# Kernel tuning notes

Hardware: AMD Instinct MI355X
Metric: run time of the kernel (lower is better)

## Reference

```python
import jax, jax.numpy as jnp
import numpy as np

N = 100000
E = 1600000
IN_DIM = 64
HID = 64


def _glorot(key, shape):
    fan_in, fan_out = shape[0], shape[1]
    lim = np.sqrt(6.0 / (fan_in + fan_out))
    return jax.random.uniform(key, shape, jnp.float32, -lim, lim)


def setup_inputs() -> dict:
    key = jax.random.key(0)
    ks = jax.random.split(key, 14)
    x = jax.random.normal(ks[0], (N, IN_DIM), jnp.float32)
    edge_index = jax.random.randint(ks[1], (2, E), 0, N, jnp.int64)
    dims = [(IN_DIM, HID), (HID, HID), (HID, HID), (HID, 1)]
    inp = {"x": x, "edge_index": edge_index}
    for i, (di, do) in enumerate(dims, start=1):
        inp[f"Wself{i}"] = _glorot(ks[2 + 3 * (i - 1)], (di, do))
        inp[f"Wneigh{i}"] = _glorot(ks[3 + 3 * (i - 1)], (di, do))
        inp[f"b{i}"] = jnp.zeros((do,), jnp.float32)
    return inp


def _gn_block(h, src, dst, deg_inv, Wself, Wneigh, b, act):
    # gather -> scatter-add -> mean -> dense transform (GraphConv-style)
    msg = h[src]                                           # [E, d]
    agg = jax.ops.segment_sum(msg, dst, num_segments=N)    # [N, d]
    agg = agg * deg_inv                                    # mean aggregation
    out = h @ Wself + agg @ Wneigh + b
    return act(out)


def reference(x, edge_index, Wself1, Wneigh1, b1, Wself2, Wneigh2, b2,
              Wself3, Wneigh3, b3, Wself4, Wneigh4, b4):
    src, dst = edge_index[0], edge_index[1]
    deg = jax.ops.segment_sum(jnp.ones((E,), x.dtype), dst, num_segments=N)
    deg_inv = (1.0 / jnp.maximum(deg, 1.0))[:, None]       # [N, 1]
    relu = jax.nn.relu
    h = _gn_block(x, src, dst, deg_inv, Wself1, Wneigh1, b1, relu)
    h = _gn_block(h, src, dst, deg_inv, Wself2, Wneigh2, b2, relu)
    h = _gn_block(h, src, dst, deg_inv, Wself3, Wneigh3, b3, relu)
    h = _gn_block(h, src, dst, deg_inv, Wself4, Wneigh4, b4, lambda z: z)
    return jax.nn.sigmoid(h)                               # [N, 1]
```

## Files before the change

### kernel.cpp

```cpp
#include <hip/hip_runtime.h>
#include <hip/hip_bf16.h>
#include <math.h>


using bfrag = __attribute__((ext_vector_type(8))) short;
using ffrag = __attribute__((ext_vector_type(4))) float;

#define BKT_SHIFT 7
#define BKT_NODES (1 << BKT_SHIFT)

__device__ __forceinline__ int load_idx32(const int* __restrict__ ei32, int is64,
                                          long long pos) {
    return is64 ? ei32[2 * pos] : ei32[pos];
}

__device__ __forceinline__ unsigned short f2b_rne(float f) {
    union { float f; unsigned u; } c;
    c.f = f;
    unsigned r = c.u + 0x7FFFu + ((c.u >> 16) & 1u);
    return (unsigned short)(r >> 16);
}

__device__ __forceinline__ float b2f(unsigned short u) {
    union { unsigned u; float f; } c;
    c.u = ((unsigned)u) << 16;
    return c.f;
}

__global__ void prep_kernel(
    const float* __restrict__ Ws1, const float* __restrict__ Wn1,
    const float* __restrict__ Ws2, const float* __restrict__ Wn2,
    const float* __restrict__ Ws3, const float* __restrict__ Wn3,
    unsigned short* __restrict__ bthi, unsigned short* __restrict__ btlo,
    const int* __restrict__ ei, int* __restrict__ bktc, int* __restrict__ flag,
    const float4* __restrict__ x4, ushort4* __restrict__ hi4, int n4) {
    int bid = blockIdx.x;
    if (bid < 96) {
        if (bid < 4) bktc[bid * 256 + threadIdx.x] = 0;
        if (bid == 0 && threadIdx.x == 0) {
            int allz = 1;
            for (int i = 0; i < 32; ++i)
                if (ei[2 * i + 1] != 0) allz = 0;
            *flag = allz;
        }
        int i = bid * 256 + threadIdx.x;
        if (i < 3 * 8192) {
            int layer = i >> 13;
            int j = i & 8191;
            int n = j >> 7, k = j & 127;
            const float* Ws = layer == 0 ? Ws1 : (layer == 1 ? Ws2 : Ws3);
            const float* Wn = layer == 0 ? Wn1 : (layer == 1 ? Wn2 : Wn3);
            float v = (k < 64) ? Ws[k * 64 + n] : Wn[(k - 64) * 64 + n];
            unsigned short hi = f2b_rne(v);
            bthi[i] = hi;
            btlo[i] = f2b_rne(v - b2f(hi));
        }
    } else {
        int i = (bid - 96) * 256 + threadIdx.x;
        if (i < n4) {
            float4 v = x4[i];
            ushort4 h;
            h.x = f2b_rne(v.x); h.y = f2b_rne(v.y);
            h.z = f2b_rne(v.z); h.w = f2b_rne(v.w);
            hi4[i] = h;
        }
    }
}

__global__ __launch_bounds__(256) void binA_kernel(
    const int* __restrict__ ei32, const int* __restrict__ flagp,
    int* __restrict__ bktCnt, unsigned* __restrict__ bins, int E, int nbkt,
    int cap, int chunksz) {
    __shared__ int cnt[1024];
    __shared__ int base[1024];
    int is64 = *flagp;
    int elo = blockIdx.x * chunksz;
    int ehi = min(E, elo + chunksz);
    if (elo >= E) return;
    for (int i = threadIdx.x; i < nbkt; i += 256) cnt[i] = 0;
    __syncthreads();
    for (int e = elo + (int)threadIdx.x; e < ehi; e += 256) {
        int dst = load_idx32(ei32, is64, (long long)E + e);
        atomicAdd(&cnt[dst >> BKT_SHIFT], 1);
    }
    __syncthreads();
    for (int i = threadIdx.x; i < nbkt; i += 256) {
        base[i] = atomicAdd(&bktCnt[i], cnt[i]);
        cnt[i] = 0;
    }
    __syncthreads();
    for (int e = elo + (int)threadIdx.x; e < ehi; e += 256) {
        int dst = load_idx32(ei32, is64, (long long)E + e);
        int src = load_idx32(ei32, is64, e);
        int b = dst >> BKT_SHIFT;
        int r = atomicAdd(&cnt[b], 1);
        bins[(size_t)b * cap + base[b] + r] =
            ((unsigned)(dst & (BKT_NODES - 1)) << 24) | (unsigned)src;
    }
}

__global__ __launch_bounds__(256) void bucketCSR_kernel(
    const int* __restrict__ bktCnt, const unsigned* __restrict__ bins,
    int* __restrict__ off, int* __restrict__ offe, int* __restrict__ col,
    float* __restrict__ dinv, int N, int cap) {
    __shared__ int deg[BKT_NODES];
    __shared__ int loc[BKT_NODES];
    __shared__ int ssum[BKT_NODES];
    int b = blockIdx.x;
    int lo = b << BKT_SHIFT;
    int n = min(BKT_NODES, N - lo);
    int t = threadIdx.x;
    if (t < BKT_NODES) deg[t] = 0;
    __syncthreads();
    int cnt = bktCnt[b];
    const unsigned* bb = bins + (size_t)b * cap;
    for (int i = t; i < cnt; i += 256)
        atomicAdd(&deg[bb[i] >> 24], 1);
    __syncthreads();
    if (t < BKT_NODES) ssum[t] = deg[t];
    __syncthreads();
    for (int o = 1; o < BKT_NODES; o <<= 1) {
        int v = (t >= o && t < BKT_NODES) ? ssum[t - o] : 0;
        __syncthreads();
        if (t < BKT_NODES) ssum[t] += v;
        __syncthreads();
    }
    if (t < BKT_NODES) loc[t] = ssum[t] - deg[t];
    __syncthreads();
    int base = b * cap;
    if (t < n) {
        int d = deg[t];
        off[lo + t] = base + loc[t];
        offe[lo + t] = base + loc[t] + d;
        dinv[lo + t] = 1.0f / fmaxf((float)d, 1.0f);
    }
    __syncthreads();
    for (int i = t; i < cnt; i += 256) {
        unsigned p = bb[i];
        int pos = atomicAdd(&loc[p >> 24], 1);
        col[base + pos] = (int)(p & 0xFFFFFFu);
    }
}

__global__ __launch_bounds__(256) void gather64_b16_kernel(
    const unsigned short* __restrict__ hb, const int* __restrict__ off,
    const int* __restrict__ offe, const int* __restrict__ col,
    const float* __restrict__ dinv, unsigned short* __restrict__ ghi, int N) {
    int wave = threadIdx.x >> 6;
    int lane = threadIdx.x & 63;
    int g = lane >> 4;
    int t = lane & 15;
    int n = blockIdx.x * 4 + wave;
    if (n >= N) return;
    int e = off[n], end = offe[n];
    float4 a0 = make_float4(0.f, 0.f, 0.f, 0.f);
    float4 a1 = make_float4(0.f, 0.f, 0.f, 0.f);
    float4 a2 = make_float4(0.f, 0.f, 0.f, 0.f);
    float4 a3 = make_float4(0.f, 0.f, 0.f, 0.f);
    for (; e + 16 <= end; e += 16) {
        int s0 = col[e + g];
        int s1 = col[e + 4 + g];
        int s2 = col[e + 8 + g];
        int s3 = col[e + 12 + g];
        ushort4 u0 = *(const ushort4*)&hb[(size_t)s0 * 64 + t * 4];
        ushort4 u1 = *(const ushort4*)&hb[(size_t)s1 * 64 + t * 4];
        ushort4 u2 = *(const ushort4*)&hb[(size_t)s2 * 64 + t * 4];
        ushort4 u3 = *(const ushort4*)&hb[(size_t)s3 * 64 + t * 4];
        a0.x += b2f(u0.x); a0.y += b2f(u0.y); a0.z += b2f(u0.z); a0.w += b2f(u0.w);
        a1.x += b2f(u1.x); a1.y += b2f(u1.y); a1.z += b2f(u1.z); a1.w += b2f(u1.w);
        a2.x += b2f(u2.x); a2.y += b2f(u2.y); a2.z += b2f(u2.z); a2.w += b2f(u2.w);
        a3.x += b2f(u3.x); a3.y += b2f(u3.y); a3.z += b2f(u3.z); a3.w += b2f(u3.w);
    }
    for (; e + 8 <= end; e += 8) {
        int s0 = col[e + g];
        int s1 = col[e + 4 + g];
        ushort4 u0 = *(const ushort4*)&hb[(size_t)s0 * 64 + t * 4];
        ushort4 u1 = *(const ushort4*)&hb[(size_t)s1 * 64 + t * 4];
        a0.x += b2f(u0.x); a0.y += b2f(u0.y); a0.z += b2f(u0.z); a0.w += b2f(u0.w);
        a1.x += b2f(u1.x); a1.y += b2f(u1.y); a1.z += b2f(u1.z); a1.w += b2f(u1.w);
    }
    for (; e < end; e += 4) {
        if (e + g < end) {
            int s0 = col[e + g];
            ushort4 u0 = *(const ushort4*)&hb[(size_t)s0 * 64 + t * 4];
            a2.x += b2f(u0.x); a2.y += b2f(u0.y); a2.z += b2f(u0.z); a2.w += b2f(u0.w);
        }
    }
    float4 acc;
    acc.x = (a0.x + a1.x) + (a2.x + a3.x);
    acc.y = (a0.y + a1.y) + (a2.y + a3.y);
    acc.z = (a0.z + a1.z) + (a2.z + a3.z);
    acc.w = (a0.w + a1.w) + (a2.w + a3.w);
#pragma unroll
    for (int m = 16; m <= 32; m <<= 1) {
        acc.x += __shfl_xor(acc.x, m, 64);
        acc.y += __shfl_xor(acc.y, m, 64);
        acc.z += __shfl_xor(acc.z, m, 64);
        acc.w += __shfl_xor(acc.w, m, 64);
    }
    if (g == 0) {
        float di = dinv[n];
        ushort4 h;
        h.x = f2b_rne(acc.x * di);
        h.y = f2b_rne(acc.y * di);
        h.z = f2b_rne(acc.z * di);
        h.w = f2b_rne(acc.w * di);
        *(ushort4*)&ghi[(size_t)n * 64 + t * 4] = h;
    }
}

__global__ __launch_bounds__(256) void dense_mfma_kernel(
    const unsigned short* __restrict__ Hhi, const unsigned short* __restrict__ Ghi,
    const unsigned short* __restrict__ Bthi, const unsigned short* __restrict__ Btlo,
    const float* __restrict__ b, unsigned short* __restrict__ Dhi, int N) {
    int lane = threadIdx.x & 63;
    int m = lane & 15, quad = lane >> 4;
    int wid = (blockIdx.x * blockDim.x + threadIdx.x) >> 6;
    int nw = (gridDim.x * blockDim.x) >> 6;
    bfrag bhi[4][4];
#pragma unroll
    for (int t = 0; t < 4; ++t)
#pragma unroll
        for (int c = 0; c < 4; ++c)
            bhi[t][c] = *(const bfrag*)(Bthi + (size_t)(t * 16 + m) * 128 + c * 32 + quad * 8);
    float bl[4];
#pragma unroll
    for (int t = 0; t < 4; ++t) bl[t] = b[t * 16 + m];
    int ngroups = (N + 15) >> 4;
    for (int g = wid; g < ngroups; g += nw) {
        int n0 = g << 4;
        int nr = n0 + m;
        if (nr > N - 1) nr = N - 1;
        const unsigned short* hrow = Hhi + (size_t)nr * 64 + quad * 8;
        const unsigned short* grow = Ghi + (size_t)nr * 64 + quad * 8;
        bfrag ah[4];
        ah[0] = *(const bfrag*)(hrow);
        ah[1] = *(const bfrag*)(hrow + 32);
        ah[2] = *(const bfrag*)(grow);
        ah[3] = *(const bfrag*)(grow + 32);
#pragma unroll
        for (int t = 0; t < 4; ++t) {
            ffrag acc = {bl[t], bl[t], bl[t], bl[t]};
#pragma unroll
            for (int c = 0; c < 4; ++c) {
                bfrag blo = *(const bfrag*)(Btlo + (size_t)(t * 16 + m) * 128 + c * 32 + quad * 8);
                acc = __builtin_amdgcn_mfma_f32_16x16x32_bf16(ah[c], bhi[t][c], acc, 0, 0, 0);
                acc = __builtin_amdgcn_mfma_f32_16x16x32_bf16(ah[c], blo, acc, 0, 0, 0);
            }
#pragma unroll
            for (int r = 0; r < 4; ++r) {
                int node = n0 + quad * 4 + r;
                if (node < N)
                    Dhi[(size_t)node * 64 + t * 16 + m] = f2b_rne(fmaxf(acc[r], 0.f));
            }
        }
    }
}

__global__ __launch_bounds__(256) void dense_mfma_last_kernel(
    const unsigned short* __restrict__ Hhi, const unsigned short* __restrict__ Ghi,
    const unsigned short* __restrict__ Bthi, const unsigned short* __restrict__ Btlo,
    const float* __restrict__ b, const float* __restrict__ Ws4,
    const float* __restrict__ Wn4, float* __restrict__ sbuf,
    float* __restrict__ gbuf, int N) {
    int lane = threadIdx.x & 63;
    int m = lane & 15, quad = lane >> 4;
    int wid = (blockIdx.x * blockDim.x + threadIdx.x) >> 6;
    int nw = (gridDim.x * blockDim.x) >> 6;
    bfrag bhi[4][4];
#pragma unroll
    for (int t = 0; t < 4; ++t)
#pragma unroll
        for (int c = 0; c < 4; ++c)
            bhi[t][c] = *(const bfrag*)(Bthi + (size_t)(t * 16 + m) * 128 + c * 32 + quad * 8);
    float bl[4], w4s[4], w4n[4];
#pragma unroll
    for (int t = 0; t < 4; ++t) {
        bl[t] = b[t * 16 + m];
        w4s[t] = Ws4[t * 16 + m];
        w4n[t] = Wn4[t * 16 + m];
    }
    int ngroups = (N + 15) >> 4;
    for (int g = wid; g < ngroups; g += nw) {
        int n0 = g << 4;
        int nr = n0 + m;
        if (nr > N - 1) nr = N - 1;
        const unsigned short* hrow = Hhi + (size_t)nr * 64 + quad * 8;
        const unsigned short* grow = Ghi + (size_t)nr * 64 + quad * 8;
        bfrag ah[4];
        ah[0] = *(const bfrag*)(hrow);
        ah[1] = *(const bfrag*)(hrow + 32);
        ah[2] = *(const bfrag*)(grow);
        ah[3] = *(const bfrag*)(grow + 32);
        ffrag accs[4];
#pragma unroll
        for (int t = 0; t < 4; ++t) {
            ffrag acc = {bl[t], bl[t], bl[t], bl[t]};
#pragma unroll
            for (int c = 0; c < 4; ++c) {
                bfrag blo = *(const bfrag*)(Btlo + (size_t)(t * 16 + m) * 128 + c * 32 + quad * 8);
                acc = __builtin_amdgcn_mfma_f32_16x16x32_bf16(ah[c], bhi[t][c], acc, 0, 0, 0);
                acc = __builtin_amdgcn_mfma_f32_16x16x32_bf16(ah[c], blo, acc, 0, 0, 0);
            }
            accs[t] = acc;
        }
#pragma unroll
        for (int r = 0; r < 4; ++r) {
            float ps = 0.f, pg = 0.f;
#pragma unroll
            for (int t = 0; t < 4; ++t) {
                float v = fmaxf(accs[t][r], 0.f);
                ps = fmaf(v, w4s[t], ps);
                pg = fmaf(v, w4n[t], pg);
            }
#pragma unroll
            for (int mask = 1; mask <= 8; mask <<= 1) {
                ps += __shfl_xor(ps, mask, 64);
                pg += __shfl_xor(pg, mask, 64);
            }
            int node = n0 + quad * 4 + r;
            if (m == 0 && node < N) {
                sbuf[node] = ps;
                gbuf[node] = pg;
            }
        }
    }
}

__global__ void final_kernel(const float* __restrict__ s, const float* __restrict__ dinv,
                             const float* __restrict__ g, const int* __restrict__ off,
                             const int* __restrict__ offe, const int* __restrict__ col,
                             const float* __restrict__ b4, float* __restrict__ out, int N) {
    int n = blockIdx.x * blockDim.x + threadIdx.x;
    if (n >= N) return;
    float a = 0.f;
    int e = off[n], end = offe[n];
    for (; e < end; ++e) a += g[col[e]];
    float z = s[n] + dinv[n] * a + b4[0];
    out[n] = 1.0f / (1.0f + expf(-z));
}

static inline int cdiv(long long a, long long b) { return (int)((a + b - 1) / b); }

extern "C" void kernel_launch(void* const* d_in, const int* in_sizes, int n_in,
                              void* d_out, int out_size, void* d_ws, size_t ws_size,
                              hipStream_t stream) {
    const float* x   = (const float*)d_in[0];
    const int*   ei  = (const int*)d_in[1];
    const float* Ws1 = (const float*)d_in[2];
    const float* Wn1 = (const float*)d_in[3];
    const float* b1  = (const float*)d_in[4];
    const float* Ws2 = (const float*)d_in[5];
    const float* Wn2 = (const float*)d_in[6];
    const float* b2  = (const float*)d_in[7];
    const float* Ws3 = (const float*)d_in[8];
    const float* Wn3 = (const float*)d_in[9];
    const float* b3  = (const float*)d_in[10];
    const float* Ws4 = (const float*)d_in[11];
    const float* Wn4 = (const float*)d_in[12];
    const float* b4  = (const float*)d_in[13];
    float* out = (float*)d_out;

    const int N = in_sizes[0] / 64;
    const int E = in_sizes[1] / 2;

    const int nbkt = cdiv(N, BKT_NODES);
    const int cap  = E / nbkt + E / nbkt / 8 + 64;

    unsigned* bins = (unsigned*)d_ws;
    int* col = (int*)(bins + (size_t)nbkt * cap);
    unsigned short* HhiA = (unsigned short*)(col + (size_t)nbkt * cap);
    unsigned short* HhiB = HhiA + (size_t)N * 64;
    unsigned short* Ghi  = HhiB + (size_t)N * 64;
    unsigned short* Bth  = Ghi + (size_t)N * 64;
    unsigned short* Btl  = Bth + 3 * 8192;
    float* dinv = (float*)(Btl + 3 * 8192);
    float* sbuf = dinv + N;
    float* gbuf = sbuf + N;
    int*   off  = (int*)(gbuf + N);
    int*   offe = off + N;
    int*   bktc = offe + N;
    int*   flag = bktc + 1024;

    const int BT = 256;
    const int gridN  = cdiv(N, BT);
    const int gridNd = cdiv(N, 4);
    const int gridMM = cdiv(cdiv(N, 16), 4);
    const int binBlocks = 256;
    const int chunksz = cdiv(E, binBlocks);
    const int gridPrep = 96 + cdiv((long long)N * 16, BT);

    prep_kernel<<<gridPrep, BT, 0, stream>>>(Ws1, Wn1, Ws2, Wn2, Ws3, Wn3,
                                             Bth, Btl, ei, bktc, flag,
                                             (const float4*)x, (ushort4*)HhiA, N * 16);

    binA_kernel<<<binBlocks, BT, 0, stream>>>(ei, flag, bktc, bins, E, nbkt, cap, chunksz);
    bucketCSR_kernel<<<nbkt, BT, 0, stream>>>(bktc, bins, off, offe, col, dinv, N, cap);

    gather64_b16_kernel<<<gridNd, BT, 0, stream>>>(HhiA, off, offe, col, dinv, Ghi, N);
    dense_mfma_kernel<<<gridMM, BT, 0, stream>>>(HhiA, Ghi, Bth, Btl, b1, HhiB, N);

    gather64_b16_kernel<<<gridNd, BT, 0, stream>>>(HhiB, off, offe, col, dinv, Ghi, N);
    dense_mfma_kernel<<<gridMM, BT, 0, stream>>>(HhiB, Ghi, Bth + 8192, Btl + 8192,
                                                 b2, HhiA, N);

    gather64_b16_kernel<<<gridNd, BT, 0, stream>>>(HhiA, off, offe, col, dinv, Ghi, N);
    dense_mfma_last_kernel<<<gridMM, BT, 0, stream>>>(HhiA, Ghi, Bth + 16384,
                                                      Btl + 16384, b3, Ws4, Wn4,
                                                      sbuf, gbuf, N);

    final_kernel<<<gridN, BT, 0, stream>>>(sbuf, dinv, gbuf, off, offe, col, b4, out, N);
}
```

Before: 404.9 us.

## Fuse all stages into one cooperative persistent kernel with grid syncs

Replaces the nine separate kernel launches (prep, binning, CSR build, three gather/dense pairs, final) with a single cooperative persistent kernel that separates phases with grid.sync() and uses grid-stride loops. It also stops holding the hi bf16 weight fragments in registers across the loop and reloads them per tile, which lowers register pressure so more blocks can be resident. The aim is to remove launch gaps and tail effects between stages. In exchange, parallelism is capped at the resident block count, binning uses at most 256 blocks, and the weight reloads add memory traffic.

```diff
diff --git a/kernel.cpp b/kernel.cpp
--- a/kernel.cpp
+++ b/kernel.cpp
@@ -1,6 +1,9 @@
 #include <hip/hip_runtime.h>
 #include <hip/hip_bf16.h>
+#include <hip/hip_cooperative_groups.h>
 #include <math.h>
+
+namespace cg = cooperative_groups;
 
 
 using bfrag = __attribute__((ext_vector_type(8))) short;
@@ -8,6 +11,7 @@
 
 #define BKT_SHIFT 7
 #define BKT_NODES (1 << BKT_SHIFT)
+#define BINB 256
 
 __device__ __forceinline__ int load_idx32(const int* __restrict__ ei32, int is64,
                                           long long pos) {
@@ -27,208 +31,79 @@
     return c.f;
 }
 
-__global__ void prep_kernel(
-    const float* __restrict__ Ws1, const float* __restrict__ Wn1,
-    const float* __restrict__ Ws2, const float* __restrict__ Wn2,
-    const float* __restrict__ Ws3, const float* __restrict__ Wn3,
-    unsigned short* __restrict__ bthi, unsigned short* __restrict__ btlo,
-    const int* __restrict__ ei, int* __restrict__ bktc, int* __restrict__ flag,
-    const float4* __restrict__ x4, ushort4* __restrict__ hi4, int n4) {
-    int bid = blockIdx.x;
-    if (bid < 96) {
-        if (bid < 4) bktc[bid * 256 + threadIdx.x] = 0;
-        if (bid == 0 && threadIdx.x == 0) {
-            int allz = 1;
-            for (int i = 0; i < 32; ++i)
-                if (ei[2 * i + 1] != 0) allz = 0;
-            *flag = allz;
-        }
-        int i = bid * 256 + threadIdx.x;
-        if (i < 3 * 8192) {
-            int layer = i >> 13;
-            int j = i & 8191;
-            int n = j >> 7, k = j & 127;
-            const float* Ws = layer == 0 ? Ws1 : (layer == 1 ? Ws2 : Ws3);
-            const float* Wn = layer == 0 ? Wn1 : (layer == 1 ? Wn2 : Wn3);
-            float v = (k < 64) ? Ws[k * 64 + n] : Wn[(k - 64) * 64 + n];
-            unsigned short hi = f2b_rne(v);
-            bthi[i] = hi;
-            btlo[i] = f2b_rne(v - b2f(hi));
-        }
-    } else {
-        int i = (bid - 96) * 256 + threadIdx.x;
-        if (i < n4) {
-            float4 v = x4[i];
-            ushort4 h;
-            h.x = f2b_rne(v.x); h.y = f2b_rne(v.y);
-            h.z = f2b_rne(v.z); h.w = f2b_rne(v.w);
-            hi4[i] = h;
-        }
-    }
-}
-
-__global__ __launch_bounds__(256) void binA_kernel(
-    const int* __restrict__ ei32, const int* __restrict__ flagp,
-    int* __restrict__ bktCnt, unsigned* __restrict__ bins, int E, int nbkt,
-    int cap, int chunksz) {
-    __shared__ int cnt[1024];
-    __shared__ int base[1024];
-    int is64 = *flagp;
-    int elo = blockIdx.x * chunksz;
-    int ehi = min(E, elo + chunksz);
-    if (elo >= E) return;
-    for (int i = threadIdx.x; i < nbkt; i += 256) cnt[i] = 0;
-    __syncthreads();
-    for (int e = elo + (int)threadIdx.x; e < ehi; e += 256) {
-        int dst = load_idx32(ei32, is64, (long long)E + e);
-        atomicAdd(&cnt[dst >> BKT_SHIFT], 1);
-    }
-    __syncthreads();
-    for (int i = threadIdx.x; i < nbkt; i += 256) {
-        base[i] = atomicAdd(&bktCnt[i], cnt[i]);
-        cnt[i] = 0;
-    }
-    __syncthreads();
-    for (int e = elo + (int)threadIdx.x; e < ehi; e += 256) {
-        int dst = load_idx32(ei32, is64, (long long)E + e);
-        int src = load_idx32(ei32, is64, e);
-        int b = dst >> BKT_SHIFT;
-        int r = atomicAdd(&cnt[b], 1);
-        bins[(size_t)b * cap + base[b] + r] =
-            ((unsigned)(dst & (BKT_NODES - 1)) << 24) | (unsigned)src;
-    }
-}
-
-__global__ __launch_bounds__(256) void bucketCSR_kernel(
-    const int* __restrict__ bktCnt, const unsigned* __restrict__ bins,
-    int* __restrict__ off, int* __restrict__ offe, int* __restrict__ col,
-    float* __restrict__ dinv, int N, int cap) {
-    __shared__ int deg[BKT_NODES];
-    __shared__ int loc[BKT_NODES];
-    __shared__ int ssum[BKT_NODES];
-    int b = blockIdx.x;
-    int lo = b << BKT_SHIFT;
-    int n = min(BKT_NODES, N - lo);
-    int t = threadIdx.x;
-    if (t < BKT_NODES) deg[t] = 0;
-    __syncthreads();
-    int cnt = bktCnt[b];
-    const unsigned* bb = bins + (size_t)b * cap;
-    for (int i = t; i < cnt; i += 256)
-        atomicAdd(&deg[bb[i] >> 24], 1);
-    __syncthreads();
-    if (t < BKT_NODES) ssum[t] = deg[t];
-    __syncthreads();
-    for (int o = 1; o < BKT_NODES; o <<= 1) {
-        int v = (t >= o && t < BKT_NODES) ? ssum[t - o] : 0;
-        __syncthreads();
-        if (t < BKT_NODES) ssum[t] += v;
-        __syncthreads();
-    }
-    if (t < BKT_NODES) loc[t] = ssum[t] - deg[t];
-    __syncthreads();
-    int base = b * cap;
-    if (t < n) {
-        int d = deg[t];
-        off[lo + t] = base + loc[t];
-        offe[lo + t] = base + loc[t] + d;
-        dinv[lo + t] = 1.0f / fmaxf((float)d, 1.0f);
-    }
-    __syncthreads();
-    for (int i = t; i < cnt; i += 256) {
-        unsigned p = bb[i];
-        int pos = atomicAdd(&loc[p >> 24], 1);
-        col[base + pos] = (int)(p & 0xFFFFFFu);
-    }
-}
-
-__global__ __launch_bounds__(256) void gather64_b16_kernel(
+__device__ __forceinline__ void gather_phase(
     const unsigned short* __restrict__ hb, const int* __restrict__ off,
     const int* __restrict__ offe, const int* __restrict__ col,
-    const float* __restrict__ dinv, unsigned short* __restrict__ ghi, int N) {
-    int wave = threadIdx.x >> 6;
-    int lane = threadIdx.x & 63;
-    int g = lane >> 4;
-    int t = lane & 15;
-    int n = blockIdx.x * 4 + wave;
-    if (n >= N) return;
-    int e = off[n], end = offe[n];
-    float4 a0 = make_float4(0.f, 0.f, 0.f, 0.f);
-    float4 a1 = make_float4(0.f, 0.f, 0.f, 0.f);
-    float4 a2 = make_float4(0.f, 0.f, 0.f, 0.f);
-    float4 a3 = make_float4(0.f, 0.f, 0.f, 0.f);
-    for (; e + 16 <= end; e += 16) {
-        int s0 = col[e + g];
-        int s1 = col[e + 4 + g];
-        int s2 = col[e + 8 + g];
-        int s3 = col[e + 12 + g];
-        ushort4 u0 = *(const ushort4*)&hb[(size_t)s0 * 64 + t * 4];
-        ushort4 u1 = *(const ushort4*)&hb[(size_t)s1 * 64 + t * 4];
-        ushort4 u2 = *(const ushort4*)&hb[(size_t)s2 * 64 + t * 4];
-        ushort4 u3 = *(const ushort4*)&hb[(size_t)s3 * 64 + t * 4];
-        a0.x += b2f(u0.x); a0.y += b2f(u0.y); a0.z += b2f(u0.z); a0.w += b2f(u0.w);
-        a1.x += b2f(u1.x); a1.y += b2f(u1.y); a1.z += b2f(u1.z); a1.w += b2f(u1.w);
-        a2.x += b2f(u2.x); a2.y += b2f(u2.y); a2.z += b2f(u2.z); a2.w += b2f(u2.w);
-        a3.x += b2f(u3.x); a3.y += b2f(u3.y); a3.z += b2f(u3.z); a3.w += b2f(u3.w);
-    }
-    for (; e + 8 <= end; e += 8) {
-        int s0 = col[e + g];
-        int s1 = col[e + 4 + g];
-        ushort4 u0 = *(const ushort4*)&hb[(size_t)s0 * 64 + t * 4];
-        ushort4 u1 = *(const ushort4*)&hb[(size_t)s1 * 64 + t * 4];
-        a0.x += b2f(u0.x); a0.y += b2f(u0.y); a0.z += b2f(u0.z); a0.w += b2f(u0.w);
-        a1.x += b2f(u1.x); a1.y += b2f(u1.y); a1.z += b2f(u1.z); a1.w += b2f(u1.w);
-    }
-    for (; e < end; e += 4) {
-        if (e + g < end) {
+    const float* __restrict__ dinv, unsigned short* __restrict__ ghi,
+    int N, int wid, int nw, int g, int t) {
+    for (int n = wid; n < N; n += nw) {
+        int e = off[n], end = offe[n];
+        float4 a0 = make_float4(0.f, 0.f, 0.f, 0.f);
+        float4 a1 = make_float4(0.f, 0.f, 0.f, 0.f);
+        float4 a2 = make_float4(0.f, 0.f, 0.f, 0.f);
+        float4 a3 = make_float4(0.f, 0.f, 0.f, 0.f);
+        for (; e + 16 <= end; e += 16) {
             int s0 = col[e + g];
+            int s1 = col[e + 4 + g];
+            int s2 = col[e + 8 + g];
+            int s3 = col[e + 12 + g];
             ushort4 u0 = *(const ushort4*)&hb[(size_t)s0 * 64 + t * 4];
-            a2.x += b2f(u0.x); a2.y += b2f(u0.y); a2.z += b2f(u0.z); a2.w += b2f(u0.w);
-        }
-    }
-    float4 acc;
-    acc.x = (a0.x + a1.x) + (a2.x + a3.x);
-    acc.y = (a0.y + a1.y) + (a2.y + a3.y);
-    acc.z = (a0.z + a1.z) + (a2.z + a3.z);
-    acc.w = (a0.w + a1.w) + (a2.w + a3.w);
-#pragma unroll
-    for (int m = 16; m <= 32; m <<= 1) {
-        acc.x += __shfl_xor(acc.x, m, 64);
-        acc.y += __shfl_xor(acc.y, m, 64);
-        acc.z += __shfl_xor(acc.z, m, 64);
-        acc.w += __shfl_xor(acc.w, m, 64);
-    }
-    if (g == 0) {
-        float di = dinv[n];
-        ushort4 h;
-        h.x = f2b_rne(acc.x * di);
-        h.y = f2b_rne(acc.y * di);
-        h.z = f2b_rne(acc.z * di);
-        h.w = f2b_rne(acc.w * di);
-        *(ushort4*)&ghi[(size_t)n * 64 + t * 4] = h;
-    }
-}
-
-__global__ __launch_bounds__(256) void dense_mfma_kernel(
+            ushort4 u1 = *(const ushort4*)&hb[(size_t)s1 * 64 + t * 4];
+            ushort4 u2 = *(const ushort4*)&hb[(size_t)s2 * 64 + t * 4];
+            ushort4 u3 = *(const ushort4*)&hb[(size_t)s3 * 64 + t * 4];
+            a0.x += b2f(u0.x); a0.y += b2f(u0.y); a0.z += b2f(u0.z); a0.w += b2f(u0.w);
+            a1.x += b2f(u1.x); a1.y += b2f(u1.y); a1.z += b2f(u1.z); a1.w += b2f(u1.w);
+            a2.x += b2f(u2.x); a2.y += b2f(u2.y); a2.z += b2f(u2.z); a2.w += b2f(u2.w);
+            a3.x += b2f(u3.x); a3.y += b2f(u3.y); a3.z += b2f(u3.z); a3.w += b2f(u3.w);
+        }
+        for (; e + 8 <= end; e += 8) {
+            int s0 = col[e + g];
+            int s1 = col[e + 4 + g];
+            ushort4 u0 = *(const ushort4*)&hb[(size_t)s0 * 64 + t * 4];
+            ushort4 u1 = *(const ushort4*)&hb[(size_t)s1 * 64 + t * 4];
+            a0.x += b2f(u0.x); a0.y += b2f(u0.y); a0.z += b2f(u0.z); a0.w += b2f(u0.w);
+            a1.x += b2f(u1.x); a1.y += b2f(u1.y); a1.z += b2f(u1.z); a1.w += b2f(u1.w);
+        }
+        for (; e < end; e += 4) {
+            if (e + g < end) {
+                int s0 = col[e + g];
+                ushort4 u0 = *(const ushort4*)&hb[(size_t)s0 * 64 + t * 4];
+                a2.x += b2f(u0.x); a2.y += b2f(u0.y); a2.z += b2f(u0.z); a2.w += b2f(u0.w);
+            }
+        }
+        float4 acc;
+        acc.x = (a0.x + a1.x) + (a2.x + a3.x);
+        acc.y = (a0.y + a1.y) + (a2.y + a3.y);
+        acc.z = (a0.z + a1.z) + (a2.z + a3.z);
+        acc.w = (a0.w + a1.w) + (a2.w + a3.w);
+#pragma unroll
+        for (int m = 16; m <= 32; m <<= 1) {
+            acc.x += __shfl_xor(acc.x, m, 64);
+            acc.y += __shfl_xor(acc.y, m, 64);
+            acc.z += __shfl_xor(acc.z, m, 64);
+            acc.w += __shfl_xor(acc.w, m, 64);
+        }
+        if (g == 0) {
+            float di = dinv[n];
+            ushort4 h;
+            h.x = f2b_rne(acc.x * di);
+            h.y = f2b_rne(acc.y * di);
+            h.z = f2b_rne(acc.z * di);
+            h.w = f2b_rne(acc.w * di);
+            *(ushort4*)&ghi[(size_t)n * 64 + t * 4] = h;
+        }
+    }
+}
+
+__device__ __forceinline__ void dense_phase(
     const unsigned short* __restrict__ Hhi, const unsigned short* __restrict__ Ghi,
     const unsigned short* __restrict__ Bthi, const unsigned short* __restrict__ Btlo,
-    const float* __restrict__ b, unsigned short* __restrict__ Dhi, int N) {
-    int lane = threadIdx.x & 63;
+    const float* __restrict__ b, unsigned short* __restrict__ Dhi,
+    int N, int wid, int nw, int lane) {
     int m = lane & 15, quad = lane >> 4;
-    int wid = (blockIdx.x * blockDim.x + threadIdx.x) >> 6;
-    int nw = (gridDim.x * blockDim.x) >> 6;
-    bfrag bhi[4][4];
-#pragma unroll
-    for (int t = 0; t < 4; ++t)
-#pragma unroll
-        for (int c = 0; c < 4; ++c)
-            bhi[t][c] = *(const bfrag*)(Bthi + (size_t)(t * 16 + m) * 128 + c * 32 + quad * 8);
-    float bl[4];
-#pragma unroll
-    for (int t = 0; t < 4; ++t) bl[t] = b[t * 16 + m];
     int ngroups = (N + 15) >> 4;
-    for (int g = wid; g < ngroups; g += nw) {
-        int n0 = g << 4;
+    for (int gg = wid; gg < ngroups; gg += nw) {
+        int n0 = gg << 4;
         int nr = n0 + m;
         if (nr > N - 1) nr = N - 1;
         const unsigned short* hrow = Hhi + (size_t)nr * 64 + quad * 8;
@@ -240,12 +115,14 @@
         ah[3] = *(const bfrag*)(grow + 32);
 #pragma unroll
         for (int t = 0; t < 4; ++t) {
-            ffrag acc = {bl[t], bl[t], bl[t], bl[t]};
+            float bl = b[t * 16 + m];
+            ffrag acc = {bl, bl, bl, bl};
 #pragma unroll
             for (int c = 0; c < 4; ++c) {
-                bfrag blo = *(const bfrag*)(Btlo + (size_t)(t * 16 + m) * 128 + c * 32 + quad * 8);
-                acc = __builtin_amdgcn_mfma_f32_16x16x32_bf16(ah[c], bhi[t][c], acc, 0, 0, 0);
-                acc = __builtin_amdgcn_mfma_f32_16x16x32_bf16(ah[c], blo, acc, 0, 0, 0);
+                bfrag bh = *(const bfrag*)(Bthi + (size_t)(t * 16 + m) * 128 + c * 32 + quad * 8);
+                bfrag bw = *(const bfrag*)(Btlo + (size_t)(t * 16 + m) * 128 + c * 32 + quad * 8);
+                acc = __builtin_amdgcn_mfma_f32_16x16x32_bf16(ah[c], bh, acc, 0, 0, 0);
+                acc = __builtin_amdgcn_mfma_f32_16x16x32_bf16(ah[c], bw, acc, 0, 0, 0);
             }
 #pragma unroll
             for (int r = 0; r < 4; ++r) {
@@ -257,32 +134,16 @@
     }
 }
 
-__global__ __launch_bounds__(256) void dense_mfma_last_kernel(
+__device__ __forceinline__ void dense_last_phase(
     const unsigned short* __restrict__ Hhi, const unsigned short* __restrict__ Ghi,
     const unsigned short* __restrict__ Bthi, const unsigned short* __restrict__ Btlo,
     const float* __restrict__ b, const float* __restrict__ Ws4,
     const float* __restrict__ Wn4, float* __restrict__ sbuf,
-    float* __restrict__ gbuf, int N) {
-    int lane = threadIdx.x & 63;
+    float* __restrict__ gbuf, int N, int wid, int nw, int lane) {
     int m = lane & 15, quad = lane >> 4;
-    int wid = (blockIdx.x * blockDim.x + threadIdx.x) >> 6;
-    int nw = (gridDim.x * blockDim.x) >> 6;
-    bfrag bhi[4][4];
-#pragma unroll
-    for (int t = 0; t < 4; ++t)
-#pragma unroll
-        for (int c = 0; c < 4; ++c)
-            bhi[t][c] = *(const bfrag*)(Bthi + (size_t)(t * 16 + m) * 128 + c * 32 + quad * 8);
-    float bl[4], w4s[4], w4n[4];
-#pragma unroll
-    for (int t = 0; t < 4; ++t) {
-        bl[t] = b[t * 16 + m];
-        w4s[t] = Ws4[t * 16 + m];
-        w4n[t] = Wn4[t * 16 + m];
-    }
     int ngroups = (N + 15) >> 4;
-    for (int g = wid; g < ngroups; g += nw) {
-        int n0 = g << 4;
+    for (int gg = wid; gg < ngroups; gg += nw) {
+        int n0 = gg << 4;
         int nr = n0 + m;
         if (nr > N - 1) nr = N - 1;
         const unsigned short* hrow = Hhi + (size_t)nr * 64 + quad * 8;
@@ -295,14 +156,22 @@
         ffrag accs[4];
 #pragma unroll
         for (int t = 0; t < 4; ++t) {
-            ffrag acc = {bl[t], bl[t], bl[t], bl[t]};
+            float bl = b[t * 16 + m];
+            ffrag acc = {bl, bl, bl, bl};
 #pragma unroll
             for (int c = 0; c < 4; ++c) {
-                bfrag blo = *(const bfrag*)(Btlo + (size_t)(t * 16 + m) * 128 + c * 32 + quad * 8);
-                acc = __builtin_amdgcn_mfma_f32_16x16x32_bf16(ah[c], bhi[t][c], acc, 0, 0, 0);
-                acc = __builtin_amdgcn_mfma_f32_16x16x32_bf16(ah[c], blo, acc, 0, 0, 0);
+                bfrag bh = *(const bfrag*)(Bthi + (size_t)(t * 16 + m) * 128 + c * 32 + quad * 8);
+                bfrag bw = *(const bfrag*)(Btlo + (size_t)(t * 16 + m) * 128 + c * 32 + quad * 8);
+                acc = __builtin_amdgcn_mfma_f32_16x16x32_bf16(ah[c], bh, acc, 0, 0, 0);
+                acc = __builtin_amdgcn_mfma_f32_16x16x32_bf16(ah[c], bw, acc, 0, 0, 0);
             }
             accs[t] = acc;
+        }
+        float w4s[4], w4n[4];
+#pragma unroll
+        for (int t = 0; t < 4; ++t) {
+            w4s[t] = Ws4[t * 16 + m];
+            w4n[t] = Wn4[t * 16 + m];
         }
 #pragma unroll
         for (int r = 0; r < 4; ++r) {
@@ -327,17 +196,157 @@
     }
 }
 
-__global__ void final_kernel(const float* __restrict__ s, const float* __restrict__ dinv,
-                             const float* __restrict__ g, const int* __restrict__ off,
-                             const int* __restrict__ offe, const int* __restrict__ col,
-                             const float* __restrict__ b4, float* __restrict__ out, int N) {
-    int n = blockIdx.x * blockDim.x + threadIdx.x;
-    if (n >= N) return;
-    float a = 0.f;
-    int e = off[n], end = offe[n];
-    for (; e < end; ++e) a += g[col[e]];
-    float z = s[n] + dinv[n] * a + b4[0];
-    out[n] = 1.0f / (1.0f + expf(-z));
+__global__ __launch_bounds__(256) void mega_kernel(
+    const float4* __restrict__ x4, const int* __restrict__ ei,
+    const float* __restrict__ Ws1, const float* __restrict__ Wn1, const float* __restrict__ b1,
+    const float* __restrict__ Ws2, const float* __restrict__ Wn2, const float* __restrict__ b2,
+    const float* __restrict__ Ws3, const float* __restrict__ Wn3, const float* __restrict__ b3,
+    const float* __restrict__ Ws4, const float* __restrict__ Wn4, const float* __restrict__ b4,
+    float* __restrict__ out,
+    unsigned* __restrict__ bins, int* __restrict__ col,
+    unsigned short* __restrict__ HhiA, unsigned short* __restrict__ HhiB,
+    unsigned short* __restrict__ Ghi, unsigned short* __restrict__ Bth,
+    unsigned short* __restrict__ Btl, float* __restrict__ dinv,
+    float* __restrict__ sbuf, float* __restrict__ gbuf,
+    int* __restrict__ off, int* __restrict__ offe,
+    int* __restrict__ bktc, int* __restrict__ flag,
+    int N, int E, int nbkt, int cap) {
+    cg::grid_group grid = cg::this_grid();
+    __shared__ int smem[2048];
+    int tid = blockIdx.x * 256 + threadIdx.x;
+    int nthr = gridDim.x * 256;
+    int wid = tid >> 6;
+    int nw = nthr >> 6;
+    int lane = threadIdx.x & 63;
+    int g = lane >> 4;
+    int t16 = lane & 15;
+
+    for (int i = tid; i < 3 * 8192; i += nthr) {
+        int layer = i >> 13;
+        int j = i & 8191;
+        int n = j >> 7, k = j & 127;
+        const float* Ws = layer == 0 ? Ws1 : (layer == 1 ? Ws2 : Ws3);
+        const float* Wn = layer == 0 ? Wn1 : (layer == 1 ? Wn2 : Wn3);
+        float v = (k < 64) ? Ws[k * 64 + n] : Wn[(k - 64) * 64 + n];
+        unsigned short hi = f2b_rne(v);
+        Bth[i] = hi;
+        Btl[i] = f2b_rne(v - b2f(hi));
+    }
+    for (int i = tid; i < N * 16; i += nthr) {
+        float4 v = x4[i];
+        ushort4 h;
+        h.x = f2b_rne(v.x); h.y = f2b_rne(v.y);
+        h.z = f2b_rne(v.z); h.w = f2b_rne(v.w);
+        ((ushort4*)HhiA)[i] = h;
+    }
+    for (int i = tid; i < nbkt; i += nthr) bktc[i] = 0;
+    if (tid == 0) {
+        int allz = 1;
+        for (int i = 0; i < 32; ++i)
+            if (ei[2 * i + 1] != 0) allz = 0;
+        *flag = allz;
+    }
+    grid.sync();
+
+    {
+        int binb = min((int)gridDim.x, BINB);
+        if ((int)blockIdx.x < binb) {
+            int* cnt = smem;
+            int* base = smem + 1024;
+            int is64 = *flag;
+            int chunksz = (E + binb - 1) / binb;
+            int elo = blockIdx.x * chunksz;
+            int ehi = min(E, elo + chunksz);
+            if (elo < E) {
+                for (int i = threadIdx.x; i < nbkt; i += 256) cnt[i] = 0;
+                __syncthreads();
+                for (int e = elo + (int)threadIdx.x; e < ehi; e += 256) {
+                    int dst = load_idx32(ei, is64, (long long)E + e);
+                    atomicAdd(&cnt[dst >> BKT_SHIFT], 1);
+                }
+                __syncthreads();
+                for (int i = threadIdx.x; i < nbkt; i += 256) {
+                    base[i] = atomicAdd(&bktc[i], cnt[i]);
+                    cnt[i] = 0;
+                }
+                __syncthreads();
+                for (int e = elo + (int)threadIdx.x; e < ehi; e += 256) {
+                    int dst = load_idx32(ei, is64, (long long)E + e);
+                    int src = load_idx32(ei, is64, e);
+                    int b = dst >> BKT_SHIFT;
+                    int r = atomicAdd(&cnt[b], 1);
+                    bins[(size_t)b * cap + base[b] + r] =
+                        ((unsigned)(dst & (BKT_NODES - 1)) << 24) | (unsigned)src;
+                }
+            }
+        }
+    }
+    grid.sync();
+
+    for (int b = blockIdx.x; b < nbkt; b += gridDim.x) {
+        int* deg = smem;
+        int* loc = smem + BKT_NODES;
+        int* ssum = smem + 2 * BKT_NODES;
+        int lo = b << BKT_SHIFT;
+        int n = min(BKT_NODES, N - lo);
+        int t = threadIdx.x;
+        if (t < BKT_NODES) deg[t] = 0;
+        __syncthreads();
+        int cnt = bktc[b];
+        const unsigned* bb = bins + (size_t)b * cap;
+        for (int i = t; i < cnt; i += 256)
+            atomicAdd(&deg[bb[i] >> 24], 1);
+        __syncthreads();
+        if (t < BKT_NODES) ssum[t] = deg[t];
+        __syncthreads();
+        for (int o = 1; o < BKT_NODES; o <<= 1) {
+            int v = (t >= o && t < BKT_NODES) ? ssum[t - o] : 0;
+            __syncthreads();
+            if (t < BKT_NODES) ssum[t] += v;
+            __syncthreads();
+        }
+        if (t < BKT_NODES) loc[t] = ssum[t] - deg[t];
+        __syncthreads();
+        int base = b * cap;
+        if (t < n) {
+            int d = deg[t];
+            off[lo + t] = base + loc[t];
+            offe[lo + t] = base + loc[t] + d;
+            dinv[lo + t] = 1.0f / fmaxf((float)d, 1.0f);
+        }
+        __syncthreads();
+        for (int i = t; i < cnt; i += 256) {
+            unsigned p = bb[i];
+            int pos = atomicAdd(&loc[p >> 24], 1);
+            col[base + pos] = (int)(p & 0xFFFFFFu);
+        }
+        __syncthreads();
+    }
+    grid.sync();
+
+    gather_phase(HhiA, off, offe, col, dinv, Ghi, N, wid, nw, g, t16);
+    grid.sync();
+    dense_phase(HhiA, Ghi, Bth, Btl, b1, HhiB, N, wid, nw, lane);
+    grid.sync();
+
+    gather_phase(HhiB, off, offe, col, dinv, Ghi, N, wid, nw, g, t16);
+    grid.sync();
+    dense_phase(HhiB, Ghi, Bth + 8192, Btl + 8192, b2, HhiA, N, wid, nw, lane);
+    grid.sync();
+
+    gather_phase(HhiA, off, offe, col, dinv, Ghi, N, wid, nw, g, t16);
+    grid.sync();
+    dense_last_phase(HhiA, Ghi, Bth + 16384, Btl + 16384, b3, Ws4, Wn4,
+                     sbuf, gbuf, N, wid, nw, lane);
+    grid.sync();
+
+    for (int n = tid; n < N; n += nthr) {
+        float a = 0.f;
+        int e = off[n], end = offe[n];
+        for (; e < end; ++e) a += gbuf[col[e]];
+        float z = sbuf[n] + dinv[n] * a + b4[0];
+        out[n] = 1.0f / (1.0f + expf(-z));
+    }
 }
 
 static inline int cdiv(long long a, long long b) { return (int)((a + b - 1) / b); }
@@ -361,11 +370,10 @@
     const float* b4  = (const float*)d_in[13];
     float* out = (float*)d_out;
 
-    const int N = in_sizes[0] / 64;
-    const int E = in_sizes[1] / 2;
-
-    const int nbkt = cdiv(N, BKT_NODES);
-    const int cap  = E / nbkt + E / nbkt / 8 + 64;
+    int N = in_sizes[0] / 64;
+    int E = in_sizes[1] / 2;
+    int nbkt = cdiv(N, BKT_NODES);
+    int cap  = E / nbkt + E / nbkt / 8 + 64;
 
     unsigned* bins = (unsigned*)d_ws;
     int* col = (int*)(bins + (size_t)nbkt * cap);
@@ -382,32 +390,27 @@
     int*   bktc = offe + N;
     int*   flag = bktc + 1024;
 
-    const int BT = 256;
-    const int gridN  = cdiv(N, BT);
-    const int gridNd = cdiv(N, 4);
-    const int gridMM = cdiv(cdiv(N, 16), 4);
-    const int binBlocks = 256;
-    const int chunksz = cdiv(E, binBlocks);
-    const int gridPrep = 96 + cdiv((long long)N * 16, BT);
-
-    prep_kernel<<<gridPrep, BT, 0, stream>>>(Ws1, Wn1, Ws2, Wn2, Ws3, Wn3,
-                                             Bth, Btl, ei, bktc, flag,
-                                             (const float4*)x, (ushort4*)HhiA, N * 16);
-
-    binA_kernel<<<binBlocks, BT, 0, stream>>>(ei, flag, bktc, bins, E, nbkt, cap, chunksz);
-    bucketCSR_kernel<<<nbkt, BT, 0, stream>>>(bktc, bins, off, offe, col, dinv, N, cap);
-
-    gather64_b16_kernel<<<gridNd, BT, 0, stream>>>(HhiA, off, offe, col, dinv, Ghi, N);
-    dense_mfma_kernel<<<gridMM, BT, 0, stream>>>(HhiA, Ghi, Bth, Btl, b1, HhiB, N);
-
-    gather64_b16_kernel<<<gridNd, BT, 0, stream>>>(HhiB, off, offe, col, dinv, Ghi, N);
-    dense_mfma_kernel<<<gridMM, BT, 0, stream>>>(HhiB, Ghi, Bth + 8192, Btl + 8192,
-                                                 b2, HhiA, N);
-
-    gather64_b16_kernel<<<gridNd, BT, 0, stream>>>(HhiA, off, offe, col, dinv, Ghi, N);
-    dense_mfma_last_kernel<<<gridMM, BT, 0, stream>>>(HhiA, Ghi, Bth + 16384,
-                                                      Btl + 16384, b3, Ws4, Wn4,
-                                                      sbuf, gbuf, N);
-
-    final_kernel<<<gridN, BT, 0, stream>>>(sbuf, dinv, gbuf, off, offe, col, b4, out, N);
-}
+    int cus = 256, maxBlk = 4;
+    hipDeviceGetAttribute(&cus, hipDeviceAttributeMultiprocessorCount, 0);
+    hipOccupancyMaxActiveBlocksPerMultiprocessor(&maxBlk, (const void*)mega_kernel,
+                                                 256, 0);
+    if (maxBlk < 1) maxBlk = 1;
+    int gridSz = cus * maxBlk;
+
+    const float4* x4 = (const float4*)x;
+    void* args[] = {
+        (void*)&x4, (void*)&ei,
+        (void*)&Ws1, (void*)&Wn1, (void*)&b1,
+        (void*)&Ws2, (void*)&Wn2, (void*)&b2,
+        (void*)&Ws3, (void*)&Wn3, (void*)&b3,
+        (void*)&Ws4, (void*)&Wn4, (void*)&b4,
+        (void*)&out,
+        (void*)&bins, (void*)&col, (void*)&HhiA, (void*)&HhiB,
+        (void*)&Ghi, (void*)&Bth, (void*)&Btl, (void*)&dinv,
+        (void*)&sbuf, (void*)&gbuf, (void*)&off, (void*)&offe,
+        (void*)&bktc, (void*)&flag,
+        (void*)&N, (void*)&E, (void*)&nbkt, (void*)&cap,
+    };
+    hipLaunchCooperativeKernel((const void*)mega_kernel, dim3(gridSz), dim3(256),
+                               args, 0, stream);
+}
```

After: 1.113 ms. 175% more time.
